# Optimization experiments

Measured on AMD Instinct MI355X. Metric: run time of the kernel, lower is better.

Reference implementation:

```python
import jax, jax.numpy as jnp
import numpy as np

MASK_INFTY_APPROX = 1e30
B, L, D = 2, 2048, 1024
H = 16
HD = D // H  # 64
NCODE = 512


def setup_inputs() -> dict:
    key = jax.random.key(0)
    ks = jax.random.split(key, 6)
    s = 1.0 / np.sqrt(D)
    x = jax.random.normal(ks[0], (B, L, D), dtype=jnp.float32)
    Wq = jax.random.normal(ks[1], (D, D), dtype=jnp.float32) * s
    Wk = jax.random.normal(ks[2], (D, D), dtype=jnp.float32) * s
    Wv = jax.random.normal(ks[3], (D, D), dtype=jnp.float32) * s
    Wo = jax.random.normal(ks[4], (D, D), dtype=jnp.float32) * s
    codebook = jax.random.normal(ks[5], (H, NCODE, HD), dtype=jnp.float32)
    return {"x": x, "Wq": Wq, "Wk": Wk, "Wv": Wv, "Wo": Wo, "codebook": codebook}


def _vq(k, codebook):
    # k: [B,H,L,hd], codebook: [H,C,hd]
    dot = jnp.einsum('bhld,hcd->bhlc', k, codebook)
    k2 = jnp.sum(k * k, axis=-1, keepdims=True)            # [B,H,L,1]
    c2 = jnp.sum(codebook * codebook, axis=-1)             # [H,C]
    d2 = k2 - 2.0 * dot + c2[None, :, None, :]             # [B,H,L,C]
    shortcodes = jnp.argmin(d2, axis=-1)                   # [B,H,L]
    h_idx = jnp.arange(H)[None, :, None]
    c_sel = codebook[h_idx, shortcodes]                    # [B,H,L,hd]
    # straight-through quantization
    k_hat = k + jax.lax.stop_gradient(c_sel - k)
    l_commit = jnp.mean(jnp.sum((k - jax.lax.stop_gradient(c_sel)) ** 2, axis=-1))
    l_codebook = jnp.mean(jnp.sum((jax.lax.stop_gradient(k) - c_sel) ** 2, axis=-1))
    return k_hat, shortcodes, l_commit, l_codebook


def reference(x, Wq, Wk, Wv, Wo, codebook):
    q = jnp.einsum('bld,de->ble', x, Wq.T).reshape(B, L, H, HD).transpose(0, 2, 1, 3)
    k = jnp.einsum('bld,de->ble', x, Wk.T).reshape(B, L, H, HD).transpose(0, 2, 1, 3)
    v = jnp.einsum('bld,de->ble', x, Wv.T).reshape(B, L, H, HD).transpose(0, 2, 1, 3)
    k_hat, shortcodes, l_commit, l_codebook = _vq(k, codebook)
    scale = HD ** (-0.5)
    logits = jnp.einsum('bhld,bhtd->bhlt', q, k_hat) * scale  # [B,H,L,L]
    causal_mask = jnp.tril(jnp.ones((L, L), dtype=bool))
    logits = jnp.where(causal_mask[None, None], logits, -MASK_INFTY_APPROX)
    w = jax.nn.softmax(logits, axis=-1)
    attn = jnp.einsum('bhlt,bhtd->bhld', w, v)
    attn = attn.transpose(0, 2, 1, 3).reshape(B, L, D)
    out = jnp.einsum('bld,de->ble', attn, Wo.T)
    return out, l_commit, l_codebook, shortcodes
```

## Files before the change

kernel.cpp:

```cpp
#include <hip/hip_runtime.h>
#include <stdint.h>

#define BB 2
#define HH 16
#define LL 2048
#define DD 1024
#define HDD 64
#define NC 512

typedef __bf16 bf16x8 __attribute__((ext_vector_type(8)));
typedef float f32x4 __attribute__((ext_vector_type(4)));
typedef unsigned short u16x8 __attribute__((ext_vector_type(8)));

__device__ __forceinline__ unsigned short f2bf(float f) {
  union { float f; unsigned u; } v; v.f = f;
  unsigned u = v.u;
  u += 0x7fffu + ((u >> 16) & 1u);
  return (unsigned short)(u >> 16);
}
__device__ __forceinline__ float bf2f(unsigned short h) {
  union { unsigned u; float f; } v; v.u = ((unsigned)h) << 16;
  return v.f;
}

__device__ __forceinline__ void load_lds16(const unsigned short* g, unsigned short* l) {
  __builtin_amdgcn_global_load_lds((const __attribute__((address_space(1))) void*)g,
                                   (__attribute__((address_space(3))) void*)l, 16, 0, 0);
}

__global__ void cast_all(const float* __restrict__ x, const float* __restrict__ wq,
                         const float* __restrict__ wk, const float* __restrict__ wv,
                         const float* __restrict__ wo, const float* __restrict__ cb,
                         unsigned short* __restrict__ xb, unsigned short* __restrict__ xl,
                         unsigned short* __restrict__ wb, unsigned short* __restrict__ wkl,
                         unsigned short* __restrict__ wob, unsigned short* __restrict__ cbb,
                         unsigned short* __restrict__ cbl, float* __restrict__ lsum) {
  long i = (long)blockIdx.x * blockDim.x + threadIdx.x;
  if (i == 0) lsum[0] = 0.f;
  const long NX = 4194304, NW = 1048576, NCB = 524288;
  const long TOT = NX + 4 * NW + NCB;
  for (long t = i; t < TOT; t += (long)gridDim.x * blockDim.x) {
    if (t < NX) {
      float v = x[t];
      unsigned short hi = f2bf(v);
      xb[t] = hi;
      xl[t] = f2bf(v - bf2f(hi));
    } else if (t < NX + NW) {
      wb[t - NX] = f2bf(wq[t - NX]);
    } else if (t < NX + 2 * NW) {
      long idx = t - NX - NW;
      float v = wk[idx];
      unsigned short hi = f2bf(v);
      wb[NW + idx] = hi;
      wkl[idx] = f2bf(v - bf2f(hi));
    } else if (t < NX + 3 * NW) {
      wb[t - NX] = f2bf(wv[t - NX - 2 * NW]);
    } else if (t < NX + 4 * NW) {
      wob[t - NX - 3 * NW] = f2bf(wo[t - NX - 3 * NW]);
    } else {
      long idx = t - NX - 4 * NW;
      float v = cb[idx];
      unsigned short hi = f2bf(v);
      cbb[idx] = hi;
      cbl[idx] = f2bf(v - bf2f(hi));
    }
  }
}

__global__ void c2_kernel(const float* __restrict__ cb, float* __restrict__ c2) {
  int i = blockIdx.x * blockDim.x + threadIdx.x;
  if (i >= HH * NC) return;
  const float* r = cb + (long)i * HDD;
  double s = 0.0;
  for (int j = 0; j < HDD; j++) s += (double)r[j] * (double)r[j];
  c2[i] = (float)s;
}

__global__ __launch_bounds__(256) void gemm_qv(
    const unsigned short* __restrict__ xb, const unsigned short* __restrict__ wb,
    unsigned short* __restrict__ qb, unsigned short* __restrict__ vt) {
  __shared__ __align__(16) unsigned short As[128 * 32];
  __shared__ __align__(16) unsigned short Bs[128 * 32];
  int tid = threadIdx.x;
  int wave = tid >> 6, lane = tid & 63;
  int quad = lane >> 4, col = lane & 15;
  int m0 = blockIdx.y * 128;
  int n0 = blockIdx.x * 128 + (blockIdx.x >= 8 ? 1024 : 0);
  f32x4 acc[4][4] = {};
  int row_in = (wave << 4) + (lane >> 2);
  int seg = lane & 3;
  const unsigned short* gA0 = xb + (long)(m0 + row_in) * DD + seg * 8;
  const unsigned short* gA1 = xb + (long)(m0 + 64 + row_in) * DD + seg * 8;
  const unsigned short* gB0 = wb + (long)(n0 + row_in) * DD + seg * 8;
  const unsigned short* gB1 = wb + (long)(n0 + 64 + row_in) * DD + seg * 8;
  unsigned short* lA0 = As + wave * 512;
  unsigned short* lA1 = As + 2048 + wave * 512;
  unsigned short* lB0 = Bs + wave * 512;
  unsigned short* lB1 = Bs + 2048 + wave * 512;
  int wm = wave & 1, wn = wave >> 1;
  const unsigned short* pa = As + (wm * 64 + col) * 32 + quad * 8;
  const unsigned short* pb = Bs + (wn * 64 + col) * 32 + quad * 8;
  for (int kk = 0; kk < DD; kk += 32) {
    __syncthreads();
    load_lds16(gA0 + kk, lA0);
    load_lds16(gA1 + kk, lA1);
    load_lds16(gB0 + kk, lB0);
    load_lds16(gB1 + kk, lB1);
    __syncthreads();
    bf16x8 af[4], bfr[4];
    for (int t = 0; t < 4; t++) af[t]  = *(const bf16x8*)(pa + t * 512);
    for (int t = 0; t < 4; t++) bfr[t] = *(const bf16x8*)(pb + t * 512);
    for (int mt = 0; mt < 4; mt++)
      for (int nt = 0; nt < 4; nt++)
        acc[mt][nt] = __builtin_amdgcn_mfma_f32_16x16x32_bf16(af[mt], bfr[nt], acc[mt][nt], 0, 0, 0);
  }
  for (int mt = 0; mt < 4; mt++)
    for (int nt = 0; nt < 4; nt++) {
      int mbase = m0 + wm * 64 + mt * 16 + quad * 4;
      int n = n0 + wn * 64 + nt * 16 + col;
      int which = n >> 10, e = n & 1023;
      int h = e >> 6, hd = e & 63;
      for (int r = 0; r < 4; r++) {
        int m = mbase + r;
        int b = m >> 11, l = m & 2047;
        unsigned short val = f2bf(acc[mt][nt][r]);
        long bh = (long)(b * HH + h);
        if (which == 0)      qb[(bh * LL + l) * HDD + hd] = val;
        else                 vt[(bh * HDD + hd) * LL + l] = val;
      }
    }
}

__global__ __launch_bounds__(256) void kvq(
    const unsigned short* __restrict__ xb, const unsigned short* __restrict__ xl,
    const unsigned short* __restrict__ wb, const unsigned short* __restrict__ wkl,
    const float* __restrict__ cb, const float* __restrict__ c2,
    const unsigned short* __restrict__ cbb, const unsigned short* __restrict__ cbl,
    unsigned short* __restrict__ khat, float* __restrict__ scodes,
    float* __restrict__ lsum) {
  __shared__ __align__(16) char smem[55808];
  unsigned short* Ah = (unsigned short*)smem;
  unsigned short* Al = (unsigned short*)(smem + 8192);
  unsigned short* Bh = (unsigned short*)(smem + 16384);
  unsigned short* Bl = (unsigned short*)(smem + 20480);
  float* kfL = (float*)smem;
  unsigned short* CbHb = (unsigned short*)(smem + 34816);
  unsigned short* CbLb = (unsigned short*)(smem + 44032);
  float* Cs = (float*)(smem + 53248);
  int* finalIdx = (int*)(smem + 55296);

  int tid = threadIdx.x;
  int wave = tid >> 6, lane = tid & 63;
  int quad = lane >> 4, col = lane & 15;
  int id = blockIdx.y * 16 + blockIdx.x;
  int xcd = id & 7, sidx = id >> 3;
  int mt4 = xcd * 4 + (sidx >> 4);
  int h = sidx & 15;
  int m0 = mt4 * 128;
  int n0 = h * 64;
  int bgl = m0 >> 11;
  int l0 = m0 & 2047;
  long bh = (long)(bgl * HH + h);

  Cs[tid] = c2[h * NC + tid];
  Cs[tid + 256] = c2[h * NC + 256 + tid];

  f32x4 acc[4][2] = {};
  int row_in = (wave << 4) + (lane >> 2);
  int seg = lane & 3;
  const unsigned short* gAh0 = xb + (long)(m0 + row_in) * DD + seg * 8;
  const unsigned short* gAh1 = xb + (long)(m0 + 64 + row_in) * DD + seg * 8;
  const unsigned short* gAl0 = xl + (long)(m0 + row_in) * DD + seg * 8;
  const unsigned short* gAl1 = xl + (long)(m0 + 64 + row_in) * DD + seg * 8;
  const unsigned short* gBh  = wb + (long)(1048576 + (long)(n0 + row_in) * DD) + seg * 8;
  const unsigned short* gBl  = wkl + (long)(n0 + row_in) * DD + seg * 8;
  unsigned short* lAh0 = Ah + wave * 512;
  unsigned short* lAh1 = Ah + 2048 + wave * 512;
  unsigned short* lAl0 = Al + wave * 512;
  unsigned short* lAl1 = Al + 2048 + wave * 512;
  unsigned short* lBh  = Bh + wave * 512;
  unsigned short* lBl  = Bl + wave * 512;
  int wm = wave & 1, wn = wave >> 1;
  const unsigned short* pah = Ah + (wm * 64 + col) * 32 + quad * 8;
  const unsigned short* pal = Al + (wm * 64 + col) * 32 + quad * 8;
  const unsigned short* pbh = Bh + (wn * 32 + col) * 32 + quad * 8;
  const unsigned short* pbl = Bl + (wn * 32 + col) * 32 + quad * 8;
  for (int kk = 0; kk < DD; kk += 32) {
    __syncthreads();
    load_lds16(gAh0 + kk, lAh0);
    load_lds16(gAh1 + kk, lAh1);
    load_lds16(gAl0 + kk, lAl0);
    load_lds16(gAl1 + kk, lAl1);
    load_lds16(gBh + kk, lBh);
    load_lds16(gBl + kk, lBl);
    __syncthreads();
    bf16x8 ah[4], al[4], bhf[2], blf[2];
    for (int t = 0; t < 4; t++) ah[t] = *(const bf16x8*)(pah + t * 512);
    for (int t = 0; t < 4; t++) al[t] = *(const bf16x8*)(pal + t * 512);
    for (int t = 0; t < 2; t++) bhf[t] = *(const bf16x8*)(pbh + t * 512);
    for (int t = 0; t < 2; t++) blf[t] = *(const bf16x8*)(pbl + t * 512);
    for (int mt = 0; mt < 4; mt++)
      for (int nt = 0; nt < 2; nt++) {
        acc[mt][nt] = __builtin_amdgcn_mfma_f32_16x16x32_bf16(ah[mt], bhf[nt], acc[mt][nt], 0, 0, 0);
        acc[mt][nt] = __builtin_amdgcn_mfma_f32_16x16x32_bf16(ah[mt], blf[nt], acc[mt][nt], 0, 0, 0);
        acc[mt][nt] = __builtin_amdgcn_mfma_f32_16x16x32_bf16(al[mt], bhf[nt], acc[mt][nt], 0, 0, 0);
      }
  }
  __syncthreads();
  const unsigned short* cbbh = cbb + (long)h * NC * HDD;
  const unsigned short* cblh = cbl + (long)h * NC * HDD;
  int srow = tid >> 3;
  int sseg = (tid & 7) * 8;
  const unsigned short* gH = cbbh + (long)srow * HDD + sseg;
  const unsigned short* gL = cblh + (long)srow * HDD + sseg;
  int ldsOff = srow * 72 + sseg;
  u16x8 ph0 = *(const u16x8*)(gH);
  u16x8 pl0 = *(const u16x8*)(gL);
  for (int mt = 0; mt < 4; mt++)
    for (int nt = 0; nt < 2; nt++) {
      int rbasew = wm * 64 + mt * 16 + quad * 4;
      int hd = wn * 32 + nt * 16 + col;
      for (int r = 0; r < 4; r++)
        kfL[(rbasew + r) * 68 + hd] = acc[mt][nt][r];
    }
  *(u16x8*)(CbHb + ldsOff) = ph0;
  *(u16x8*)(CbLb + ldsOff) = pl0;
  __syncthreads();

  bf16x8 bfh[2][2], bfl[2][2];
  float k2g[2];
#pragma unroll
  for (int g = 0; g < 2; g++) {
    const float* kp = kfL + (wave * 32 + g * 16 + col) * 68 + quad * 8;
    float4 t0 = *(const float4*)(kp);
    float4 t1 = *(const float4*)(kp + 4);
    float4 t2 = *(const float4*)(kp + 32);
    float4 t3 = *(const float4*)(kp + 36);
    float fv[16];
    fv[0]=t0.x; fv[1]=t0.y; fv[2]=t0.z; fv[3]=t0.w;
    fv[4]=t1.x; fv[5]=t1.y; fv[6]=t1.z; fv[7]=t1.w;
    fv[8]=t2.x; fv[9]=t2.y; fv[10]=t2.z; fv[11]=t2.w;
    fv[12]=t3.x; fv[13]=t3.y; fv[14]=t3.z; fv[15]=t3.w;
    float k2 = 0.f;
#pragma unroll
    for (int j = 0; j < 16; j++) k2 = fmaf(fv[j], fv[j], k2);
    k2 += __shfl_xor(k2, 16);
    k2 += __shfl_xor(k2, 32);
    k2g[g] = k2;
    u16x8 h0, h1, l0u, l1u;
#pragma unroll
    for (int j = 0; j < 8; j++) {
      unsigned short hi = f2bf(fv[j]);
      h0[j] = hi; l0u[j] = f2bf(fv[j] - bf2f(hi));
      unsigned short hi2 = f2bf(fv[8 + j]);
      h1[j] = hi2; l1u[j] = f2bf(fv[8 + j] - bf2f(hi2));
    }
    bfh[g][0] = __builtin_bit_cast(bf16x8, h0);
    bfh[g][1] = __builtin_bit_cast(bf16x8, h1);
    bfl[g][0] = __builtin_bit_cast(bf16x8, l0u);
    bfl[g][1] = __builtin_bit_cast(bf16x8, l1u);
  }
  float b1v[2] = {1e38f, 1e38f}, b2v[2] = {1e38f, 1e38f};
  int b1i[2] = {0x7fffffff, 0x7fffffff}, b2i[2] = {0x7fffffff, 0x7fffffff};
  for (int t = 0; t < 16; t++) {
    int cur = t & 1;
    u16x8 nh, nl;
    if (t < 15) {
      nh = *(const u16x8*)(gH + (t + 1) * 32 * HDD);
      nl = *(const u16x8*)(gL + (t + 1) * 32 * HDD);
    }
    const unsigned short* CbHc = CbHb + cur * 2304;
    const unsigned short* CbLc = CbLb + cur * 2304;
#pragma unroll
    for (int s = 0; s < 2; s++) {
      const unsigned short* rp = CbHc + (s * 16 + col) * 72 + quad * 8;
      const unsigned short* rq = CbLc + (s * 16 + col) * 72 + quad * 8;
      bf16x8 ah0 = *(const bf16x8*)(rp);
      bf16x8 ah1 = *(const bf16x8*)(rp + 32);
      bf16x8 al0 = *(const bf16x8*)(rq);
      bf16x8 al1 = *(const bf16x8*)(rq + 32);
      f32x4 aP0 = {}, aQ0 = {}, aP1 = {}, aQ1 = {};
      aP0 = __builtin_amdgcn_mfma_f32_16x16x32_bf16(ah0, bfh[0][0], aP0, 0, 0, 0);
      aQ0 = __builtin_amdgcn_mfma_f32_16x16x32_bf16(ah1, bfh[0][1], aQ0, 0, 0, 0);
      aP1 = __builtin_amdgcn_mfma_f32_16x16x32_bf16(ah0, bfh[1][0], aP1, 0, 0, 0);
      aQ1 = __builtin_amdgcn_mfma_f32_16x16x32_bf16(ah1, bfh[1][1], aQ1, 0, 0, 0);
      aP0 = __builtin_amdgcn_mfma_f32_16x16x32_bf16(al0, bfh[0][0], aP0, 0, 0, 0);
      aQ0 = __builtin_amdgcn_mfma_f32_16x16x32_bf16(al1, bfh[0][1], aQ0, 0, 0, 0);
      aP1 = __builtin_amdgcn_mfma_f32_16x16x32_bf16(al0, bfh[1][0], aP1, 0, 0, 0);
      aQ1 = __builtin_amdgcn_mfma_f32_16x16x32_bf16(al1, bfh[1][1], aQ1, 0, 0, 0);
      aP0 = __builtin_amdgcn_mfma_f32_16x16x32_bf16(ah0, bfl[0][0], aP0, 0, 0, 0);
      aQ0 = __builtin_amdgcn_mfma_f32_16x16x32_bf16(ah1, bfl[0][1], aQ0, 0, 0, 0);
      aP1 = __builtin_amdgcn_mfma_f32_16x16x32_bf16(ah0, bfl[1][0], aP1, 0, 0, 0);
      aQ1 = __builtin_amdgcn_mfma_f32_16x16x32_bf16(ah1, bfl[1][1], aQ1, 0, 0, 0);
      f32x4 c2v = *(const f32x4*)(Cs + t * 32 + s * 16 + quad * 4);
#pragma unroll
      for (int r = 0; r < 4; r++) {
        int idx = t * 32 + s * 16 + quad * 4 + r;
        float v0 = c2v[r] - 2.0f * (aP0[r] + aQ0[r]);
        if (v0 < b1v[0]) { b2v[0] = b1v[0]; b2i[0] = b1i[0]; b1v[0] = v0; b1i[0] = idx; }
        else if (v0 < b2v[0]) { b2v[0] = v0; b2i[0] = idx; }
        float v1 = c2v[r] - 2.0f * (aP1[r] + aQ1[r]);
        if (v1 < b1v[1]) { b2v[1] = b1v[1]; b2i[1] = b1i[1]; b1v[1] = v1; b1i[1] = idx; }
        else if (v1 < b2v[1]) { b2v[1] = v1; b2i[1] = idx; }
      }
    }
    if (t < 15) {
      *(u16x8*)(CbHb + (cur ^ 1) * 2304 + ldsOff) = nh;
      *(u16x8*)(CbLb + (cur ^ 1) * 2304 + ldsOff) = nl;
    }
    __syncthreads();
  }
  const float DMARG = 0.015625f;
  float partT = 0.f;
#pragma unroll
  for (int g = 0; g < 2; g++) {
    float v1 = b1v[g], v2 = b2v[g];
    int i1 = b1i[g], i2 = b2i[g];
#pragma unroll
    for (int d = 16; d <= 32; d <<= 1) {
      float o1v = __shfl_xor(v1, d); int o1i = __shfl_xor(i1, d);
      float o2v = __shfl_xor(v2, d); int o2i = __shfl_xor(i2, d);
      if (o1v < v1 || (o1v == v1 && o1i < i1)) {
        float nv; int ni;
        if (v1 < o2v || (v1 == o2v && i1 < o2i)) { nv = v1; ni = i1; }
        else { nv = o2v; ni = o2i; }
        v1 = o1v; i1 = o1i; v2 = nv; i2 = ni;
      } else {
        if (o1v < v2 || (o1v == v2 && o1i < i2)) { v2 = o1v; i2 = o1i; }
      }
    }
    bool trig = (v2 - v1 <= DMARG);
    float part;
    int widx = i1;
    if (__any(trig)) {
      const float* kpr = kfL + (wave * 32 + g * 16 + col) * 68 + quad * 8;
      float4 f0 = *(const float4*)(kpr);
      float4 f1 = *(const float4*)(kpr + 4);
      float4 f2 = *(const float4*)(kpr + 32);
      float4 f3 = *(const float4*)(kpr + 36);
      const float* c1p = cb + ((long)h * NC + i1) * HDD + quad * 8;
      const float* c2p = cb + ((long)h * NC + i2) * HDD + quad * 8;
      float4 a0 = *(const float4*)(c1p);
      float4 a1 = *(const float4*)(c1p + 4);
      float4 a2 = *(const float4*)(c1p + 32);
      float4 a3 = *(const float4*)(c1p + 36);
      float4 e0 = *(const float4*)(c2p);
      float4 e1 = *(const float4*)(c2p + 4);
      float4 e2 = *(const float4*)(c2p + 32);
      float4 e3 = *(const float4*)(c2p + 36);
      float s1 = 0.f, s2 = 0.f;
#pragma unroll
      for (int j = 0; j < 4; j++) {
        float d;
        d = ((const float*)&f0)[j] - ((const float*)&a0)[j]; s1 = fmaf(d, d, s1);
        d = ((const float*)&f1)[j] - ((const float*)&a1)[j]; s1 = fmaf(d, d, s1);
        d = ((const float*)&f2)[j] - ((const float*)&a2)[j]; s1 = fmaf(d, d, s1);
        d = ((const float*)&f3)[j] - ((const float*)&a3)[j]; s1 = fmaf(d, d, s1);
        d = ((const float*)&f0)[j] - ((const float*)&e0)[j]; s2 = fmaf(d, d, s2);
        d = ((const float*)&f1)[j] - ((const float*)&e1)[j]; s2 = fmaf(d, d, s2);
        d = ((const float*)&f2)[j] - ((const float*)&e2)[j]; s2 = fmaf(d, d, s2);
        d = ((const float*)&f3)[j] - ((const float*)&e3)[j]; s2 = fmaf(d, d, s2);
      }
      s1 += __shfl_xor(s1, 16); s1 += __shfl_xor(s1, 32);
      s2 += __shfl_xor(s2, 16); s2 += __shfl_xor(s2, 32);
      if (trig) {
        if (s2 < s1 || (s2 == s1 && i2 < i1)) { widx = i2; part = s2; }
        else { widx = i1; part = s1; }
      } else {
        part = k2g[g] + v1;
      }
    } else {
      part = k2g[g] + v1;
    }
    if (quad == 0) partT += part;
    if (lane < 16) {
      int row_local = wave * 32 + g * 16 + lane;
      scodes[bh * LL + l0 + row_local] = (float)widx;
      finalIdx[row_local] = widx;
    }
  }
  partT += __shfl_xor(partT, 1);  partT += __shfl_xor(partT, 2);
  partT += __shfl_xor(partT, 4);  partT += __shfl_xor(partT, 8);
  partT += __shfl_xor(partT, 16); partT += __shfl_xor(partT, 32);
  if (lane == 0) atomicAdd(lsum, partT);
  __syncthreads();
  {
    int r = tid >> 1, p = (tid & 1) * 32;
    int code = finalIdx[r];
    const unsigned short* src = cbb + ((long)h * NC + code) * HDD + p;
    unsigned short* dst = khat + (bh * LL + l0 + r) * HDD + p;
    *(u16x8*)(dst)      = *(const u16x8*)(src);
    *(u16x8*)(dst + 8)  = *(const u16x8*)(src + 8);
    *(u16x8*)(dst + 16) = *(const u16x8*)(src + 16);
    *(u16x8*)(dst + 24) = *(const u16x8*)(src + 24);
  }
}

__global__ __launch_bounds__(256) void attn_kernel(
    const unsigned short* __restrict__ qb, const unsigned short* __restrict__ khat,
    const unsigned short* __restrict__ vt, unsigned short* __restrict__ attnb) {
  __shared__ __align__(16) unsigned short Pbuf[4][2][16 * 72];
  __shared__ __align__(16) unsigned short Kbuf[64 * 72];
  __shared__ __align__(16) unsigned short Vbuf[64 * 72];
  int tid = threadIdx.x, wave = tid >> 6, lane = tid & 63;
  int quad = lane >> 4, col = lane & 15;
  int id = blockIdx.y * 16 + blockIdx.x;
  int xcd = id & 7, sidx = id >> 3;
  int bh = xcd * 4 + (sidx >> 4);
  int pi = sidx & 15;
  int b = bh >> 4, h = bh & 15;
  int ta = pi, tb = 31 - pi;
  int qbA = ta * 64 + wave * 16;
  int qbB = tb * 64 + wave * 16;
  const unsigned short* qrA = qb + ((long)bh * LL + qbA + col) * HDD;
  const unsigned short* qrB = qb + ((long)bh * LL + qbB + col) * HDD;
  bf16x8 aqA0 = *(const bf16x8*)(qrA + quad * 8);
  bf16x8 aqA1 = *(const bf16x8*)(qrA + 32 + quad * 8);
  bf16x8 aqB0 = *(const bf16x8*)(qrB + quad * 8);
  bf16x8 aqB1 = *(const bf16x8*)(qrB + 32 + quad * 8);
  float lA[4] = {0.f, 0.f, 0.f, 0.f}, lB[4] = {0.f, 0.f, 0.f, 0.f};
  f32x4 oA[4] = {}, oB[4] = {};
  unsigned short* PA = Pbuf[wave][0];
  unsigned short* PB = Pbuf[wave][1];
  const unsigned short* kh = khat + (long)bh * LL * HDD;
  const unsigned short* vh = vt + (long)bh * HDD * LL;
  int srow = tid >> 2, sc = (tid & 3) * 8;
  const unsigned short* gK = kh + (long)srow * HDD + sc;
  const unsigned short* gV = vh + (long)srow * LL + sc;
  unsigned short* lK = Kbuf + srow * 72 + sc;
  unsigned short* lV = Vbuf + srow * 72 + sc;
  const float SCL = 0.18033688011112042f;
  u16x8 rk0 = *(const u16x8*)(gK);
  u16x8 rk1 = *(const u16x8*)(gK + 32);
  u16x8 rv0 = *(const u16x8*)(gV);
  u16x8 rv1 = *(const u16x8*)(gV + 32);
  for (int kt = 0; kt <= tb; kt++) {
    int kbase = kt * 64;
    bool actA = (kt <= ta);
    __syncthreads();
    *(u16x8*)lK        = rk0;
    *(u16x8*)(lK + 32) = rk1;
    *(u16x8*)lV        = rv0;
    *(u16x8*)(lV + 32) = rv1;
    __syncthreads();
    if (kt < tb) {
      const unsigned short* nK = gK + (long)(kt + 1) * 64 * HDD;
      const unsigned short* nV = gV + (kt + 1) * 64;
      rk0 = *(const u16x8*)(nK);
      rk1 = *(const u16x8*)(nK + 32);
      rv0 = *(const u16x8*)(nV);
      rv1 = *(const u16x8*)(nV + 32);
    }
    f32x4 zA[4], zB[4];
    for (int nt = 0; nt < 4; nt++) {
      const unsigned short* krow = Kbuf + (nt * 16 + col) * 72;
      bf16x8 k0 = *(const bf16x8*)(krow + quad * 8);
      bf16x8 k1 = *(const bf16x8*)(krow + 32 + quad * 8);
      f32x4 z = {};
      z = __builtin_amdgcn_mfma_f32_16x16x32_bf16(aqB0, k0, z, 0, 0, 0);
      z = __builtin_amdgcn_mfma_f32_16x16x32_bf16(aqB1, k1, z, 0, 0, 0);
      zB[nt] = z;
      if (actA) {
        f32x4 y = {};
        y = __builtin_amdgcn_mfma_f32_16x16x32_bf16(aqA0, k0, y, 0, 0, 0);
        y = __builtin_amdgcn_mfma_f32_16x16x32_bf16(aqA1, k1, y, 0, 0, 0);
        zA[nt] = y;
      }
    }
    for (int nt = 0; nt < 4; nt++) {
      int key = kbase + nt * 16 + col;
      for (int r = 0; r < 4; r++) {
        float sc2 = zB[nt][r] * SCL;
        if (kt == tb && key > qbB + quad * 4 + r) sc2 = -1e30f;
        float p = exp2f(sc2);
        lB[r] += p;
        PB[(quad * 4 + r) * 72 + nt * 16 + col] = __builtin_bit_cast(unsigned short, (__bf16)p);
      }
    }
    if (actA) {
      for (int nt = 0; nt < 4; nt++) {
        int key = kbase + nt * 16 + col;
        for (int r = 0; r < 4; r++) {
          float sc2 = zA[nt][r] * SCL;
          if (kt == ta && key > qbA + quad * 4 + r) sc2 = -1e30f;
          float p = exp2f(sc2);
          lA[r] += p;
          PA[(quad * 4 + r) * 72 + nt * 16 + col] = __builtin_bit_cast(unsigned short, (__bf16)p);
        }
      }
    }
    bf16x8 apB0 = *(const bf16x8*)(PB + col * 72 + quad * 8);
    bf16x8 apB1 = *(const bf16x8*)(PB + col * 72 + 32 + quad * 8);
    bf16x8 apA0, apA1;
    if (actA) {
      apA0 = *(const bf16x8*)(PA + col * 72 + quad * 8);
      apA1 = *(const bf16x8*)(PA + col * 72 + 32 + quad * 8);
    }
    for (int nt = 0; nt < 4; nt++) {
      const unsigned short* vrow = Vbuf + (nt * 16 + col) * 72;
      bf16x8 v0 = *(const bf16x8*)(vrow + quad * 8);
      bf16x8 v1 = *(const bf16x8*)(vrow + 32 + quad * 8);
      oB[nt] = __builtin_amdgcn_mfma_f32_16x16x32_bf16(apB0, v0, oB[nt], 0, 0, 0);
      oB[nt] = __builtin_amdgcn_mfma_f32_16x16x32_bf16(apB1, v1, oB[nt], 0, 0, 0);
      if (actA) {
        oA[nt] = __builtin_amdgcn_mfma_f32_16x16x32_bf16(apA0, v0, oA[nt], 0, 0, 0);
        oA[nt] = __builtin_amdgcn_mfma_f32_16x16x32_bf16(apA1, v1, oA[nt], 0, 0, 0);
      }
    }
  }
  float invA[4], invB[4];
  for (int r = 0; r < 4; r++) {
    float t = lA[r];
    t += __shfl_xor(t, 1); t += __shfl_xor(t, 2);
    t += __shfl_xor(t, 4); t += __shfl_xor(t, 8);
    invA[r] = 1.0f / t;
    float u = lB[r];
    u += __shfl_xor(u, 1); u += __shfl_xor(u, 2);
    u += __shfl_xor(u, 4); u += __shfl_xor(u, 8);
    invB[r] = 1.0f / u;
  }
  for (int r = 0; r < 4; r++) {
    int rowA = qbA + quad * 4 + r;
    int rowB = qbB + quad * 4 + r;
    for (int nt = 0; nt < 4; nt++) {
      int hd = nt * 16 + col;
      attnb[((long)b * LL + rowA) * DD + h * HDD + hd] = f2bf(oA[nt][r] * invA[r]);
      attnb[((long)b * LL + rowB) * DD + h * HDD + hd] = f2bf(oB[nt][r] * invB[r]);
    }
  }
}

__global__ __launch_bounds__(256) void gemm_out(
    const unsigned short* __restrict__ attnb, const unsigned short* __restrict__ wob,
    float* __restrict__ out) {
  __shared__ __align__(16) unsigned short As[128 * 32];
  __shared__ __align__(16) unsigned short Bs[128 * 32];
  int tid = threadIdx.x;
  int wave = tid >> 6, lane = tid & 63;
  int quad = lane >> 4, col = lane & 15;
  int m0 = blockIdx.y * 128;
  int n0 = blockIdx.x * 128;
  f32x4 acc[4][4] = {};
  int row_in = (wave << 4) + (lane >> 2);
  int seg = lane & 3;
  const unsigned short* gA0 = attnb + (long)(m0 + row_in) * DD + seg * 8;
  const unsigned short* gA1 = attnb + (long)(m0 + 64 + row_in) * DD + seg * 8;
  const unsigned short* gB0 = wob + (long)(n0 + row_in) * DD + seg * 8;
  const unsigned short* gB1 = wob + (long)(n0 + 64 + row_in) * DD + seg * 8;
  unsigned short* lA0 = As + wave * 512;
  unsigned short* lA1 = As + 2048 + wave * 512;
  unsigned short* lB0 = Bs + wave * 512;
  unsigned short* lB1 = Bs + 2048 + wave * 512;
  int wm = wave & 1, wn = wave >> 1;
  const unsigned short* pa = As + (wm * 64 + col) * 32 + quad * 8;
  const unsigned short* pb = Bs + (wn * 64 + col) * 32 + quad * 8;
  for (int kk = 0; kk < DD; kk += 32) {
    __syncthreads();
    load_lds16(gA0 + kk, lA0);
    load_lds16(gA1 + kk, lA1);
    load_lds16(gB0 + kk, lB0);
    load_lds16(gB1 + kk, lB1);
    __syncthreads();
    bf16x8 af[4], bfr[4];
    for (int t = 0; t < 4; t++) af[t]  = *(const bf16x8*)(pa + t * 512);
    for (int t = 0; t < 4; t++) bfr[t] = *(const bf16x8*)(pb + t * 512);
    for (int mt = 0; mt < 4; mt++)
      for (int nt = 0; nt < 4; nt++)
        acc[mt][nt] = __builtin_amdgcn_mfma_f32_16x16x32_bf16(af[mt], bfr[nt], acc[mt][nt], 0, 0, 0);
  }
  for (int mt = 0; mt < 4; mt++)
    for (int nt = 0; nt < 4; nt++) {
      int mbase = m0 + wm * 64 + mt * 16 + quad * 4;
      int n = n0 + wn * 64 + nt * 16 + col;
      for (int r = 0; r < 4; r++)
        out[(long)(mbase + r) * DD + n] = acc[mt][nt][r];
    }
}

__global__ void finalize(const float* __restrict__ lsum, float* __restrict__ out) {
  if (threadIdx.x == 0) {
    float v = lsum[0] / (float)(BB * HH * LL);
    out[4194304] = v;
    out[4194305] = v;
  }
}

extern "C" void kernel_launch(void* const* d_in, const int* in_sizes, int n_in,
                              void* d_out, int out_size, void* d_ws, size_t ws_size,
                              hipStream_t stream) {
  const float* x  = (const float*)d_in[0];
  const float* wq = (const float*)d_in[1];
  const float* wk = (const float*)d_in[2];
  const float* wv = (const float*)d_in[3];
  const float* wo = (const float*)d_in[4];
  const float* cb = (const float*)d_in[5];
  float* out = (float*)d_out;

  char* ws = (char*)d_ws;
  size_t off = 0;
  auto alloc = [&](size_t bytes) {
    void* p = ws + off;
    off = (off + bytes + 255) & ~(size_t)255;
    return p;
  };
  unsigned short* xb    = (unsigned short*)alloc(4194304 * 2);
  unsigned short* xl    = (unsigned short*)alloc(4194304 * 2);
  unsigned short* wb    = (unsigned short*)alloc(3145728 * 2);
  unsigned short* wkl   = (unsigned short*)alloc(1048576 * 2);
  unsigned short* wob   = (unsigned short*)alloc(1048576 * 2);
  unsigned short* cbb   = (unsigned short*)alloc(524288 * 2);
  unsigned short* cbl   = (unsigned short*)alloc(524288 * 2);
  unsigned short* qb    = (unsigned short*)alloc(4194304 * 2);
  unsigned short* vt    = (unsigned short*)alloc(4194304 * 2);
  unsigned short* khat  = (unsigned short*)alloc(4194304 * 2);
  unsigned short* attnb = (unsigned short*)alloc(4194304 * 2);
  float* c2   = (float*)alloc(8192 * 4);
  float* lsum = (float*)alloc(256);

  cast_all<<<dim3(4096), dim3(256), 0, stream>>>(x, wq, wk, wv, wo, cb, xb, xl, wb, wkl, wob, cbb, cbl, lsum);
  c2_kernel<<<dim3(32), dim3(256), 0, stream>>>(cb, c2);
  gemm_qv<<<dim3(16, 32), dim3(256), 0, stream>>>(xb, wb, qb, vt);
  kvq<<<dim3(16, 32), dim3(256), 0, stream>>>(xb, xl, wb, wkl, cb, c2, cbb, cbl, khat, out + 4194306, lsum);
  attn_kernel<<<dim3(16, 32), dim3(256), 0, stream>>>(qb, khat, vt, attnb);
  gemm_out<<<dim3(8, 32), dim3(256), 0, stream>>>(attnb, wob, out);
  finalize<<<dim3(1), dim3(64), 0, stream>>>(lsum, out);
}
```

Before: 300.3 us.

## Vectorize casts, drop LDS staging in VQ, transpose score MFMA for packed P stores

The cast kernel now processes four floats per thread, using float4 loads and packed u16x4 stores instead of scalar accesses. The VQ kernel reads c2 directly from global memory instead of staging it in LDS. It also gathers codebook rows by shuffling the selected indices across lanes, which removes the finalIdx LDS array and a __syncthreads. In attention, the QK^T MFMA operands are swapped so each lane owns a query row, which lets P be written with packed 4-element LDS stores and reduces the row-sum to a single scalar per lane. The risks are extra global traffic for c2 and extra shuffle work in normalization.

```diff
diff --git a/kernel.cpp b/kernel.cpp
--- a/kernel.cpp
+++ b/kernel.cpp
@@ -11,6 +11,7 @@
 typedef __bf16 bf16x8 __attribute__((ext_vector_type(8)));
 typedef float f32x4 __attribute__((ext_vector_type(4)));
 typedef unsigned short u16x8 __attribute__((ext_vector_type(8)));
+typedef unsigned short u16x4 __attribute__((ext_vector_type(4)));
 
 __device__ __forceinline__ unsigned short f2bf(float f) {
   union { float f; unsigned u; } v; v.f = f;
@@ -37,32 +38,66 @@
                          unsigned short* __restrict__ cbl, float* __restrict__ lsum) {
   long i = (long)blockIdx.x * blockDim.x + threadIdx.x;
   if (i == 0) lsum[0] = 0.f;
-  const long NX = 4194304, NW = 1048576, NCB = 524288;
-  const long TOT = NX + 4 * NW + NCB;
-  for (long t = i; t < TOT; t += (long)gridDim.x * blockDim.x) {
-    if (t < NX) {
-      float v = x[t];
-      unsigned short hi = f2bf(v);
-      xb[t] = hi;
-      xl[t] = f2bf(v - bf2f(hi));
-    } else if (t < NX + NW) {
-      wb[t - NX] = f2bf(wq[t - NX]);
-    } else if (t < NX + 2 * NW) {
-      long idx = t - NX - NW;
-      float v = wk[idx];
-      unsigned short hi = f2bf(v);
-      wb[NW + idx] = hi;
-      wkl[idx] = f2bf(v - bf2f(hi));
-    } else if (t < NX + 3 * NW) {
-      wb[t - NX] = f2bf(wv[t - NX - 2 * NW]);
-    } else if (t < NX + 4 * NW) {
-      wob[t - NX - 3 * NW] = f2bf(wo[t - NX - 3 * NW]);
+  const long NX4 = 1048576, NW4 = 262144, NCB4 = 131072;
+  const long TOT4 = NX4 + 4 * NW4 + NCB4;
+  for (long q = i; q < TOT4; q += (long)gridDim.x * blockDim.x) {
+    if (q < NX4) {
+      long t = q * 4;
+      float4 v = *(const float4*)(x + t);
+      u16x4 hi, lo;
+#pragma unroll
+      for (int j = 0; j < 4; j++) {
+        float f = ((const float*)&v)[j];
+        unsigned short h = f2bf(f);
+        hi[j] = h; lo[j] = f2bf(f - bf2f(h));
+      }
+      *(u16x4*)(xb + t) = hi;
+      *(u16x4*)(xl + t) = lo;
+    } else if (q < NX4 + NW4) {
+      long t = (q - NX4) * 4;
+      float4 v = *(const float4*)(wq + t);
+      u16x4 hi;
+#pragma unroll
+      for (int j = 0; j < 4; j++) hi[j] = f2bf(((const float*)&v)[j]);
+      *(u16x4*)(wb + t) = hi;
+    } else if (q < NX4 + 2 * NW4) {
+      long t = (q - NX4 - NW4) * 4;
+      float4 v = *(const float4*)(wk + t);
+      u16x4 hi, lo;
+#pragma unroll
+      for (int j = 0; j < 4; j++) {
+        float f = ((const float*)&v)[j];
+        unsigned short h = f2bf(f);
+        hi[j] = h; lo[j] = f2bf(f - bf2f(h));
+      }
+      *(u16x4*)(wb + 1048576 + t) = hi;
+      *(u16x4*)(wkl + t) = lo;
+    } else if (q < NX4 + 3 * NW4) {
+      long t = (q - NX4 - 2 * NW4) * 4;
+      float4 v = *(const float4*)(wv + t);
+      u16x4 hi;
+#pragma unroll
+      for (int j = 0; j < 4; j++) hi[j] = f2bf(((const float*)&v)[j]);
+      *(u16x4*)(wb + 2097152 + t) = hi;
+    } else if (q < NX4 + 4 * NW4) {
+      long t = (q - NX4 - 3 * NW4) * 4;
+      float4 v = *(const float4*)(wo + t);
+      u16x4 hi;
+#pragma unroll
+      for (int j = 0; j < 4; j++) hi[j] = f2bf(((const float*)&v)[j]);
+      *(u16x4*)(wob + t) = hi;
     } else {
-      long idx = t - NX - 4 * NW;
-      float v = cb[idx];
-      unsigned short hi = f2bf(v);
-      cbb[idx] = hi;
-      cbl[idx] = f2bf(v - bf2f(hi));
+      long t = (q - NX4 - 4 * NW4) * 4;
+      float4 v = *(const float4*)(cb + t);
+      u16x4 hi, lo;
+#pragma unroll
+      for (int j = 0; j < 4; j++) {
+        float f = ((const float*)&v)[j];
+        unsigned short h = f2bf(f);
+        hi[j] = h; lo[j] = f2bf(f - bf2f(h));
+      }
+      *(u16x4*)(cbb + t) = hi;
+      *(u16x4*)(cbl + t) = lo;
     }
   }
 }
@@ -138,7 +173,7 @@
     const unsigned short* __restrict__ cbb, const unsigned short* __restrict__ cbl,
     unsigned short* __restrict__ khat, float* __restrict__ scodes,
     float* __restrict__ lsum) {
-  __shared__ __align__(16) char smem[55808];
+  __shared__ __align__(16) char smem[53248];
   unsigned short* Ah = (unsigned short*)smem;
   unsigned short* Al = (unsigned short*)(smem + 8192);
   unsigned short* Bh = (unsigned short*)(smem + 16384);
@@ -146,8 +181,6 @@
   float* kfL = (float*)smem;
   unsigned short* CbHb = (unsigned short*)(smem + 34816);
   unsigned short* CbLb = (unsigned short*)(smem + 44032);
-  float* Cs = (float*)(smem + 53248);
-  int* finalIdx = (int*)(smem + 55296);
 
   int tid = threadIdx.x;
   int wave = tid >> 6, lane = tid & 63;
@@ -161,9 +194,7 @@
   int bgl = m0 >> 11;
   int l0 = m0 & 2047;
   long bh = (long)(bgl * HH + h);
-
-  Cs[tid] = c2[h * NC + tid];
-  Cs[tid + 256] = c2[h * NC + 256 + tid];
+  const float* c2h = c2 + h * NC;
 
   f32x4 acc[4][2] = {};
   int row_in = (wave << 4) + (lane >> 2);
@@ -292,7 +323,7 @@
       aQ0 = __builtin_amdgcn_mfma_f32_16x16x32_bf16(ah1, bfl[0][1], aQ0, 0, 0, 0);
       aP1 = __builtin_amdgcn_mfma_f32_16x16x32_bf16(ah0, bfl[1][0], aP1, 0, 0, 0);
       aQ1 = __builtin_amdgcn_mfma_f32_16x16x32_bf16(ah1, bfl[1][1], aQ1, 0, 0, 0);
-      f32x4 c2v = *(const f32x4*)(Cs + t * 32 + s * 16 + quad * 4);
+      f32x4 c2v = *(const f32x4*)(c2h + t * 32 + s * 16 + quad * 4);
 #pragma unroll
       for (int r = 0; r < 4; r++) {
         int idx = t * 32 + s * 16 + quad * 4 + r;
@@ -312,6 +343,7 @@
   }
   const float DMARG = 0.015625f;
   float partT = 0.f;
+  int w0 = 0, w1 = 0;
 #pragma unroll
   for (int g = 0; g < 2; g++) {
     float v1 = b1v[g], v2 = b2v[g];
@@ -372,23 +404,24 @@
     } else {
       part = k2g[g] + v1;
     }
+    if (g == 0) w0 = widx; else w1 = widx;
     if (quad == 0) partT += part;
-    if (lane < 16) {
-      int row_local = wave * 32 + g * 16 + lane;
-      scodes[bh * LL + l0 + row_local] = (float)widx;
-      finalIdx[row_local] = widx;
-    }
+    if (lane < 16)
+      scodes[bh * LL + l0 + wave * 32 + g * 16 + lane] = (float)widx;
   }
   partT += __shfl_xor(partT, 1);  partT += __shfl_xor(partT, 2);
   partT += __shfl_xor(partT, 4);  partT += __shfl_xor(partT, 8);
   partT += __shfl_xor(partT, 16); partT += __shfl_xor(partT, 32);
   if (lane == 0) atomicAdd(lsum, partT);
-  __syncthreads();
   {
-    int r = tid >> 1, p = (tid & 1) * 32;
-    int code = finalIdx[r];
-    const unsigned short* src = cbb + ((long)h * NC + code) * HDD + p;
-    unsigned short* dst = khat + (bh * LL + l0 + r) * HDD + p;
+    int rL = lane >> 1;
+    int srcl = rL & 15;
+    int c0 = __shfl(w0, srcl);
+    int c1 = __shfl(w1, srcl);
+    int code = (rL >> 4) ? c1 : c0;
+    int p = (lane & 1) * 32;
+    const unsigned short* src = cbbh + (long)code * HDD + p;
+    unsigned short* dst = khat + (bh * LL + l0 + wave * 32 + rL) * HDD + p;
     *(u16x8*)(dst)      = *(const u16x8*)(src);
     *(u16x8*)(dst + 8)  = *(const u16x8*)(src + 8);
     *(u16x8*)(dst + 16) = *(const u16x8*)(src + 16);
@@ -418,7 +451,7 @@
   bf16x8 aqA1 = *(const bf16x8*)(qrA + 32 + quad * 8);
   bf16x8 aqB0 = *(const bf16x8*)(qrB + quad * 8);
   bf16x8 aqB1 = *(const bf16x8*)(qrB + 32 + quad * 8);
-  float lA[4] = {0.f, 0.f, 0.f, 0.f}, lB[4] = {0.f, 0.f, 0.f, 0.f};
+  float lA = 0.f, lB = 0.f;
   f32x4 oA[4] = {}, oB[4] = {};
   unsigned short* PA = Pbuf[wave][0];
   unsigned short* PB = Pbuf[wave][1];
@@ -457,36 +490,40 @@
       bf16x8 k0 = *(const bf16x8*)(krow + quad * 8);
       bf16x8 k1 = *(const bf16x8*)(krow + 32 + quad * 8);
       f32x4 z = {};
-      z = __builtin_amdgcn_mfma_f32_16x16x32_bf16(aqB0, k0, z, 0, 0, 0);
-      z = __builtin_amdgcn_mfma_f32_16x16x32_bf16(aqB1, k1, z, 0, 0, 0);
+      z = __builtin_amdgcn_mfma_f32_16x16x32_bf16(k0, aqB0, z, 0, 0, 0);
+      z = __builtin_amdgcn_mfma_f32_16x16x32_bf16(k1, aqB1, z, 0, 0, 0);
       zB[nt] = z;
       if (actA) {
         f32x4 y = {};
-        y = __builtin_amdgcn_mfma_f32_16x16x32_bf16(aqA0, k0, y, 0, 0, 0);
-        y = __builtin_amdgcn_mfma_f32_16x16x32_bf16(aqA1, k1, y, 0, 0, 0);
+        y = __builtin_amdgcn_mfma_f32_16x16x32_bf16(k0, aqA0, y, 0, 0, 0);
+        y = __builtin_amdgcn_mfma_f32_16x16x32_bf16(k1, aqA1, y, 0, 0, 0);
         zA[nt] = y;
       }
     }
     for (int nt = 0; nt < 4; nt++) {
-      int key = kbase + nt * 16 + col;
+      u16x4 pk;
       for (int r = 0; r < 4; r++) {
         float sc2 = zB[nt][r] * SCL;
-        if (kt == tb && key > qbB + quad * 4 + r) sc2 = -1e30f;
+        int key = kbase + nt * 16 + quad * 4 + r;
+        if (kt == tb && key > qbB + col) sc2 = -1e30f;
         float p = exp2f(sc2);
-        lB[r] += p;
-        PB[(quad * 4 + r) * 72 + nt * 16 + col] = __builtin_bit_cast(unsigned short, (__bf16)p);
-      }
+        lB += p;
+        pk[r] = __builtin_bit_cast(unsigned short, (__bf16)p);
+      }
+      *(u16x4*)(PB + col * 72 + nt * 16 + quad * 4) = pk;
     }
     if (actA) {
       for (int nt = 0; nt < 4; nt++) {
-        int key = kbase + nt * 16 + col;
+        u16x4 pk;
         for (int r = 0; r < 4; r++) {
           float sc2 = zA[nt][r] * SCL;
-          if (kt == ta && key > qbA + quad * 4 + r) sc2 = -1e30f;
+          int key = kbase + nt * 16 + quad * 4 + r;
+          if (kt == ta && key > qbA + col) sc2 = -1e30f;
           float p = exp2f(sc2);
-          lA[r] += p;
-          PA[(quad * 4 + r) * 72 + nt * 16 + col] = __builtin_bit_cast(unsigned short, (__bf16)p);
+          lA += p;
+          pk[r] = __builtin_bit_cast(unsigned short, (__bf16)p);
         }
+        *(u16x4*)(PA + col * 72 + nt * 16 + quad * 4) = pk;
       }
     }
     bf16x8 apB0 = *(const bf16x8*)(PB + col * 72 + quad * 8);
@@ -508,24 +545,19 @@
       }
     }
   }
-  float invA[4], invB[4];
+  lA += __shfl_xor(lA, 16); lA += __shfl_xor(lA, 32);
+  lB += __shfl_xor(lB, 16); lB += __shfl_xor(lB, 32);
+  float invAc = 1.0f / lA;
+  float invBc = 1.0f / lB;
   for (int r = 0; r < 4; r++) {
-    float t = lA[r];
-    t += __shfl_xor(t, 1); t += __shfl_xor(t, 2);
-    t += __shfl_xor(t, 4); t += __shfl_xor(t, 8);
-    invA[r] = 1.0f / t;
-    float u = lB[r];
-    u += __shfl_xor(u, 1); u += __shfl_xor(u, 2);
-    u += __shfl_xor(u, 4); u += __shfl_xor(u, 8);
-    invB[r] = 1.0f / u;
-  }
-  for (int r = 0; r < 4; r++) {
+    float invA = __shfl(invAc, quad * 4 + r);
+    float invB = __shfl(invBc, quad * 4 + r);
     int rowA = qbA + quad * 4 + r;
     int rowB = qbB + quad * 4 + r;
     for (int nt = 0; nt < 4; nt++) {
       int hd = nt * 16 + col;
-      attnb[((long)b * LL + rowA) * DD + h * HDD + hd] = f2bf(oA[nt][r] * invA[r]);
-      attnb[((long)b * LL + rowB) * DD + h * HDD + hd] = f2bf(oB[nt][r] * invB[r]);
+      attnb[((long)b * LL + rowA) * DD + h * HDD + hd] = f2bf(oA[nt][r] * invA);
+      attnb[((long)b * LL + rowB) * DD + h * HDD + hd] = f2bf(oB[nt][r] * invB);
     }
   }
 }
```

New measurement: 290.6 us. -3.2%, faster.
